# Kernel optimization log

Measured on AMD Instinct MI355X. Metric: run time of the kernel, lower is better.

## Reference

```python
import jax, jax.numpy as jnp
import numpy as np

EMBED = 1024

def setup_inputs() -> dict:
    key = jax.random.key(0)
    ks = jax.random.split(key, 10)
    B, S, E = 4, 2048, EMBED
    inv = 1.0 / np.sqrt(E)
    return {
        "query": jax.random.normal(ks[0], (B, S, E), jnp.float32),
        "key": jax.random.normal(ks[1], (B, S, E), jnp.float32),
        "value": jax.random.normal(ks[2], (B, S, E), jnp.float32),
        "attn_mask": jnp.zeros((B, S, S), jnp.float32),
        "Wq": jax.random.normal(ks[3], (E, E), jnp.float32) * inv,
        "bq": jnp.zeros((E,), jnp.float32),
        "Wk": jax.random.normal(ks[4], (E, E), jnp.float32) * inv,
        "bk": jnp.zeros((E,), jnp.float32),
        "Wv": jax.random.normal(ks[5], (E, E), jnp.float32) * inv,
        "bv": jnp.zeros((E,), jnp.float32),
    }

def reference(query, key, value, attn_mask, Wq, bq, Wk, bk, Wv, bv):
    E = query.shape[-1]
    q = query @ Wq.T + bq            # [B,S,E]
    k = key @ Wk.T + bk              # [B,S,E]
    v = value @ Wv.T + bv            # [B,S,E]
    scores = jnp.einsum('bse,bte->bst', q, k) / jnp.sqrt(jnp.float32(E))
    scores = scores + attn_mask      # [B,S,S]
    attn = jax.nn.softmax(scores, axis=-1)
    return jnp.einsum('bst,bte->bse', attn, v)
```

## Files before the change

### kernel.cpp

```cpp
#include <hip/hip_runtime.h>
#include <cstdint>
#include <cstddef>

typedef __bf16 bf16;
typedef __bf16 bf16x8 __attribute__((ext_vector_type(8)));
typedef float  f32x4  __attribute__((ext_vector_type(4)));

#define NB 4
#define SS 2048
#define EE 1024

#define BUFB   24576
#define LDS3   (3 * BUFB)
#define BUFB64 49152
#define LDS64  (3 * BUFB64)
#define LDS64P (LDS64 + 512)

static __device__ __forceinline__ void glds16(const bf16* g, void* l)
{
    __builtin_amdgcn_global_load_lds(
        (const __attribute__((address_space(1))) unsigned int*)g,
        (__attribute__((address_space(3))) unsigned int*)l,
        16, 0, 0);
}

static __device__ __forceinline__ void swz_block(int& bx, int& by, int& bz)
{
    const int nx = gridDim.x, ny = gridDim.y;
    const int nwg = nx * ny * gridDim.z;
    int lin = blockIdx.x + nx * (blockIdx.y + ny * blockIdx.z);
    const int per = nwg >> 3;
    lin = (lin & 7) * per + (lin >> 3);
    bz = lin / (nx * ny);
    const int r = lin - bz * nx * ny;
    by = r / nx;
    bx = r - by * nx;
}

static __device__ __forceinline__ void kloop32(
    const bf16* __restrict__ A, const bf16* __restrict__ Bm,
    int lda, int ldb, int nt, char* lds, int m0, int n0, int tid,
    f32x4 acc[4][4])
{
    constexpr int NBUF = 3;
    const int lane = tid & 63, w = tid >> 6;
    const int wm = w >> 2, wn = w & 3;
    const int lr = lane & 15, kq = lane >> 4;
    const int cb = ((kq ^ ((lr >> 1) & 3)) << 4);

    const int srow   = tid >> 2;
    const int chunkL = (tid & 3) ^ ((srow >> 1) & 3);
    const bf16* Asrc = A  + (size_t)(m0 + srow) * lda + chunkL * 8;
    const bf16* Bsrc = Bm + (size_t)(n0 + srow) * ldb + chunkL * 8;
    const int wofs = w << 10;

#pragma unroll
    for (int p = 0; p < NBUF - 1; ++p) {
        char* d = lds + p * BUFB + wofs;
        const int kt = p * 32;
        glds16(Asrc + kt,                     d);
        glds16(Bsrc + kt,                     d + 8192);
        glds16(Bsrc + (size_t)128 * ldb + kt, d + 16384);
    }
    asm volatile("s_waitcnt vmcnt(3)" ::: "memory");
    __builtin_amdgcn_sched_barrier(0);
    __builtin_amdgcn_s_barrier();
    __builtin_amdgcn_sched_barrier(0);

    int rb = 0, sb = NBUF - 1;
    for (int t = 0; t < nt; ++t) {
        char* la = lds + rb * BUFB;
        char* lb = la + 8192;
        const int ts = (t + NBUF - 1 < nt) ? t + NBUF - 1 : nt - 1;
        const int kt = ts * 32;
        char* d = lds + sb * BUFB + wofs;

        bf16x8 af[4], bg[4];
#pragma unroll
        for (int m = 0; m < 4; ++m)
            af[m] = *(const bf16x8*)(la + (wm * 64 + m * 16 + lr) * 64 + cb);
#pragma unroll
        for (int n = 0; n < 4; ++n)
            bg[n] = *(const bf16x8*)(lb + (wn * 64 + n * 16 + lr) * 64 + cb);

        glds16(Asrc + kt,                     d);
        glds16(Bsrc + kt,                     d + 8192);
        glds16(Bsrc + (size_t)128 * ldb + kt, d + 16384);

        __builtin_amdgcn_s_setprio(1);
#pragma unroll
        for (int m = 0; m < 4; ++m)
#pragma unroll
            for (int n = 0; n < 4; ++n)
                acc[m][n] = __builtin_amdgcn_mfma_f32_16x16x32_bf16(af[m], bg[n], acc[m][n], 0, 0, 0);
        __builtin_amdgcn_s_setprio(0);

        if (t < nt - 1) {
            asm volatile("s_waitcnt vmcnt(3)" ::: "memory");
            __builtin_amdgcn_sched_barrier(0);
            __builtin_amdgcn_s_barrier();
            __builtin_amdgcn_sched_barrier(0);
        }
        rb = (rb + 1 == NBUF) ? 0 : rb + 1;
        sb = (sb + 1 == NBUF) ? 0 : sb + 1;
    }
    asm volatile("s_waitcnt vmcnt(0)" ::: "memory");
}

static __device__ __forceinline__ void kloop32w(
    const bf16* __restrict__ A, const bf16* __restrict__ Bm,
    int lda, int ldb, int nt, char* lds, int m0, int n0, int tid,
    f32x4 acc[4][8])
{
    constexpr int NBUF = 3;
    const int lane = tid & 63, w = tid >> 6;
    const int wm = w >> 1, wn = w & 1;
    const int lr = lane & 15, kq = lane >> 4;
    const int cb = ((kq ^ ((lr >> 1) & 3)) << 4);

    const int srow   = tid >> 2;
    const int chunkL = (tid & 3) ^ ((srow >> 1) & 3);
    const bf16* Asrc = A  + (size_t)(m0 + srow) * lda + chunkL * 8;
    const bf16* Bsrc = Bm + (size_t)(n0 + srow) * ldb + chunkL * 8;
    const int wofs = w << 10;

#pragma unroll
    for (int p = 0; p < NBUF - 1; ++p) {
        char* d = lds + p * BUFB + wofs;
        const int kt = p * 32;
        glds16(Asrc + kt,                      d);
        glds16(Asrc + (size_t)64  * lda + kt,  d + 4096);
        glds16(Bsrc + kt,                      d + 8192);
        glds16(Bsrc + (size_t)64  * ldb + kt,  d + 12288);
        glds16(Bsrc + (size_t)128 * ldb + kt,  d + 16384);
        glds16(Bsrc + (size_t)192 * ldb + kt,  d + 20480);
    }
    asm volatile("s_waitcnt vmcnt(6)" ::: "memory");
    __builtin_amdgcn_sched_barrier(0);
    __builtin_amdgcn_s_barrier();
    __builtin_amdgcn_sched_barrier(0);

    int rb = 0, sb = NBUF - 1;
    for (int t = 0; t < nt; ++t) {
        char* la = lds + rb * BUFB;
        char* lb = la + 8192;
        const int ts = (t + NBUF - 1 < nt) ? t + NBUF - 1 : nt - 1;
        const int kt = ts * 32;
        char* d = lds + sb * BUFB + wofs;

        bf16x8 af[4], bg[8];
#pragma unroll
        for (int m = 0; m < 4; ++m)
            af[m] = *(const bf16x8*)(la + (wm * 64 + m * 16 + lr) * 64 + cb);
#pragma unroll
        for (int n = 0; n < 8; ++n)
            bg[n] = *(const bf16x8*)(lb + (wn * 128 + n * 16 + lr) * 64 + cb);

        glds16(Asrc + kt,                      d);
        glds16(Asrc + (size_t)64  * lda + kt,  d + 4096);
        glds16(Bsrc + kt,                      d + 8192);
        glds16(Bsrc + (size_t)64  * ldb + kt,  d + 12288);
        glds16(Bsrc + (size_t)128 * ldb + kt,  d + 16384);
        glds16(Bsrc + (size_t)192 * ldb + kt,  d + 20480);

        __builtin_amdgcn_s_setprio(1);
#pragma unroll
        for (int m = 0; m < 4; ++m)
#pragma unroll
            for (int n = 0; n < 8; ++n)
                acc[m][n] = __builtin_amdgcn_mfma_f32_16x16x32_bf16(af[m], bg[n], acc[m][n], 0, 0, 0);
        __builtin_amdgcn_s_setprio(0);

        if (t < nt - 1) {
            asm volatile("s_waitcnt vmcnt(6)" ::: "memory");
            __builtin_amdgcn_sched_barrier(0);
            __builtin_amdgcn_s_barrier();
            __builtin_amdgcn_sched_barrier(0);
        }
        rb = (rb + 1 == NBUF) ? 0 : rb + 1;
        sb = (sb + 1 == NBUF) ? 0 : sb + 1;
    }
    asm volatile("s_waitcnt vmcnt(0)" ::: "memory");
}

static __device__ __forceinline__ void kloop64(
    const bf16* __restrict__ A, const bf16* __restrict__ Bm,
    int lda, int ldb, int nt, char* lds, int m0, int n0, int tid,
    f32x4 acc[4][4])
{
    const int lane = tid & 63, w = tid >> 6;
    const int wm = w >> 2, wn = w & 3;
    const int lr = lane & 15, kq = lane >> 4;
    const int axor = (lr & 7) << 4;

    const int srow   = tid >> 3;
    const int chunkL = (tid & 7) ^ (srow & 7);
    const bf16* Asrc = A  + (size_t)(m0 + srow) * lda + chunkL * 8;
    const bf16* Bsrc = Bm + (size_t)(n0 + srow) * ldb + chunkL * 8;
    const int wofs = w << 10;

#pragma unroll
    for (int p = 0; p < 2; ++p) {
        char* d = lds + p * BUFB64 + wofs;
        const int kt = p * 64;
        glds16(Asrc + kt,                        d);
        glds16(Asrc + (size_t)64 * lda + kt,     d + 8192);
        glds16(Bsrc + kt,                        d + 16384);
        glds16(Bsrc + (size_t)64 * ldb + kt,     d + 16384 + 8192);
        glds16(Bsrc + (size_t)128 * ldb + kt,    d + 16384 + 16384);
        glds16(Bsrc + (size_t)192 * ldb + kt,    d + 16384 + 24576);
    }
    asm volatile("s_waitcnt vmcnt(6)" ::: "memory");
    __builtin_amdgcn_sched_barrier(0);
    __builtin_amdgcn_s_barrier();
    __builtin_amdgcn_sched_barrier(0);

    for (int t = 0; t < nt; ++t) {
        char* la = lds + (t % 3) * BUFB64;
        char* lb = la + 16384;
        char* sa = lds + ((t + 2) % 3) * BUFB64;
        const bool st = (t + 2) < nt;
        const int kt = (t + 2) * 64;

        bf16x8 af[4], bg[4];
        {
            const int cbk = (kq * 16) ^ axor;
#pragma unroll
            for (int m = 0; m < 4; ++m)
                af[m] = *(const bf16x8*)(la + (wm * 64 + m * 16 + lr) * 128 + cbk);
#pragma unroll
            for (int n = 0; n < 4; ++n)
                bg[n] = *(const bf16x8*)(lb + (wn * 64 + n * 16 + lr) * 128 + cbk);
            if (st) {
                glds16(Asrc + kt,                    sa + wofs);
                glds16(Asrc + (size_t)64 * lda + kt, sa + 8192 + wofs);
                glds16(Bsrc + kt,                    sa + 16384 + wofs);
            }
            __builtin_amdgcn_s_setprio(1);
#pragma unroll
            for (int m = 0; m < 4; ++m)
#pragma unroll
                for (int n = 0; n < 4; ++n)
                    acc[m][n] = __builtin_amdgcn_mfma_f32_16x16x32_bf16(af[m], bg[n], acc[m][n], 0, 0, 0);
            __builtin_amdgcn_s_setprio(0);
        }
        {
            const int cbk = (64 + kq * 16) ^ axor;
#pragma unroll
            for (int m = 0; m < 4; ++m)
                af[m] = *(const bf16x8*)(la + (wm * 64 + m * 16 + lr) * 128 + cbk);
#pragma unroll
            for (int n = 0; n < 4; ++n)
                bg[n] = *(const bf16x8*)(lb + (wn * 64 + n * 16 + lr) * 128 + cbk);
            if (st) {
                glds16(Bsrc + (size_t)64 * ldb + kt,  sa + 16384 + 8192 + wofs);
                glds16(Bsrc + (size_t)128 * ldb + kt, sa + 16384 + 16384 + wofs);
                glds16(Bsrc + (size_t)192 * ldb + kt, sa + 16384 + 24576 + wofs);
            }
            __builtin_amdgcn_s_setprio(1);
#pragma unroll
            for (int m = 0; m < 4; ++m)
#pragma unroll
                for (int n = 0; n < 4; ++n)
                    acc[m][n] = __builtin_amdgcn_mfma_f32_16x16x32_bf16(af[m], bg[n], acc[m][n], 0, 0, 0);
            __builtin_amdgcn_s_setprio(0);
        }
        if (t < nt - 1) {
            if (st) { asm volatile("s_waitcnt vmcnt(6)" ::: "memory"); }
            else    { asm volatile("s_waitcnt vmcnt(0)" ::: "memory"); }
            __builtin_amdgcn_sched_barrier(0);
            __builtin_amdgcn_s_barrier();
            __builtin_amdgcn_sched_barrier(0);
        }
    }
}

__global__ __launch_bounds__(256) void cvt_all(
    const float* __restrict__ q, const float* __restrict__ k, const float* __restrict__ v,
    const float* __restrict__ Wq, const float* __restrict__ Wk, const float* __restrict__ Wv,
    bf16* __restrict__ qc, bf16* __restrict__ kc, bf16* __restrict__ vc,
    bf16* __restrict__ Wc)
{
    const int y = blockIdx.y;
    const float* s; bf16* d; size_t i;
    if (blockIdx.x < 4096) {
        s = (y == 0) ? q : (y == 1) ? k : v;
        d = (y == 0) ? qc : (y == 1) ? kc : vc;
        i = ((size_t)blockIdx.x * 256 + threadIdx.x) * 8;
    } else {
        s = (y == 0) ? Wq : (y == 1) ? Wk : Wv;
        d = Wc + (size_t)y * EE * EE;
        i = ((size_t)(blockIdx.x - 4096) * 256 + threadIdx.x) * 8;
    }
    const float4 f0 = *(const float4*)(s + i);
    const float4 f1 = *(const float4*)(s + i + 4);
    bf16x8 h;
    h[0] = (bf16)f0.x; h[1] = (bf16)f0.y; h[2] = (bf16)f0.z; h[3] = (bf16)f0.w;
    h[4] = (bf16)f1.x; h[5] = (bf16)f1.y; h[6] = (bf16)f1.z; h[7] = (bf16)f1.w;
    *(bf16x8*)(d + i) = h;
}

__global__ __launch_bounds__(512, 4) void proj8(
    const bf16* __restrict__ qc, const bf16* __restrict__ kc, const bf16* __restrict__ vc,
    const bf16* __restrict__ Wc,
    const float* __restrict__ bq, const float* __restrict__ bk, const float* __restrict__ bv,
    bf16* __restrict__ qb, bf16* __restrict__ kb, bf16* __restrict__ vt)
{
    extern __shared__ char lds[];
    int bx, by, bz; swz_block(bx, by, bz);
    const bf16* A; const float* bias;
    if (bz == 0)      { A = qc; bias = bq; }
    else if (bz == 1) { A = kc; bias = bk; }
    else              { A = vc; bias = bv; }
    const bf16* Bm = Wc + (size_t)bz * EE * EE;

    const int m0 = by * 128, n0 = bx * 256;
    const int tid = threadIdx.x;

    f32x4 acc[4][4];
#pragma unroll
    for (int m = 0; m < 4; ++m)
#pragma unroll
        for (int n = 0; n < 4; ++n) { acc[m][n][0] = 0.f; acc[m][n][1] = 0.f; acc[m][n][2] = 0.f; acc[m][n][3] = 0.f; }

    kloop32(A, Bm, EE, EE, EE / 32, lds, m0, n0, tid, acc);

    const int lane = tid & 63, w = tid >> 6, wm = w >> 2, wn = w & 3;
    const int lr = lane & 15, kq = lane >> 4;

    if (bz < 2) {
        bf16* out = (bz == 0) ? qb : kb;
#pragma unroll
        for (int n = 0; n < 4; ++n) {
            const int gcol = n0 + wn * 64 + n * 16 + lr;
            const float bb = bias[gcol];
#pragma unroll
            for (int m = 0; m < 4; ++m)
#pragma unroll
                for (int j = 0; j < 4; ++j) {
                    const int grow = m0 + wm * 64 + m * 16 + kq * 4 + j;
                    out[(size_t)grow * EE + gcol] = (bf16)(acc[m][n][j] + bb);
                }
        }
    } else {
        __syncthreads();
#pragma unroll
        for (int n = 0; n < 4; ++n) {
            const int gc = wn * 64 + n * 16 + lr;
            const float bb = bias[n0 + gc];
#pragma unroll
            for (int m = 0; m < 4; ++m) {
                const int gr = wm * 64 + m * 16 + kq * 4;
                union { unsigned short u[4]; uint2 v; } h;
#pragma unroll
                for (int j = 0; j < 4; ++j) {
                    union { bf16 b; unsigned short u; } cv;
                    cv.b = (bf16)(acc[m][n][j] + bb);
                    h.u[j] = cv.u;
                }
                char* p = lds + gc * 256 + (((gr >> 3) ^ (gc & 7)) << 4) + (gr & 7) * 2;
                *(uint2*)p = h.v;
            }
        }
        __syncthreads();
        const int r = tid >> 1, par = tid & 1;
        const int bb_ = m0 >> 11;
        const int s0 = m0 & (SS - 1);
        bf16* dst = vt + ((size_t)bb_ * EE + n0 + r) * SS + s0 + par * 64;
#pragma unroll
        for (int i = 0; i < 8; ++i) {
            const int c = par * 8 + i;
            const char* p = lds + r * 256 + ((c ^ (r & 7)) << 4);
            *(uint4*)&dst[i * 8] = *(const uint4*)p;
        }
    }
}

__global__ __launch_bounds__(256, 2) void scores8(const bf16* __restrict__ qb,
                                                  const bf16* __restrict__ kb,
                                                  const float* __restrict__ mask,
                                                  bf16* __restrict__ sc,
                                                  float* __restrict__ part)
{
    extern __shared__ char lds[];
    int bx, by, bz; swz_block(bx, by, bz);
    const bf16* A  = qb + (size_t)bz * SS * EE;
    const bf16* Bm = kb + (size_t)bz * SS * EE;

    const int m0 = by * 128, n0 = bx * 256;
    const int tid = threadIdx.x;

    f32x4 acc[4][8];
#pragma unroll
    for (int m = 0; m < 4; ++m)
#pragma unroll
        for (int n = 0; n < 8; ++n) { acc[m][n][0] = 0.f; acc[m][n][1] = 0.f; acc[m][n][2] = 0.f; acc[m][n][3] = 0.f; }

    kloop32w(A, Bm, EE, EE, EE / 32, lds, m0, n0, tid, acc);

    const int lane = tid & 63, w = tid >> 6, wm = w >> 1, wn = w & 1;
    const int lr = lane & 15, kq = lane >> 4;
    const float* mrow = mask + (size_t)bz * SS * SS;
    bf16* out = sc + (size_t)bz * SS * SS;
    const float scale = 0.03125f;

    float rp[4][4];
#pragma unroll
    for (int m = 0; m < 4; ++m)
#pragma unroll
        for (int j = 0; j < 4; ++j) rp[m][j] = 0.f;

#pragma unroll
    for (int m = 0; m < 4; ++m)
#pragma unroll
        for (int n = 0; n < 8; ++n)
#pragma unroll
            for (int j = 0; j < 4; ++j) {
                const int grow = m0 + wm * 64 + m * 16 + kq * 4 + j;
                const int gcol = n0 + wn * 128 + n * 16 + lr;
                const float v = acc[m][n][j] * scale + mrow[(size_t)grow * SS + gcol];
                const float e = __expf(v);
                out[(size_t)grow * SS + gcol] = (bf16)e;
                rp[m][j] += e;
            }

#pragma unroll
    for (int m = 0; m < 4; ++m)
#pragma unroll
        for (int j = 0; j < 4; ++j) {
            float s = rp[m][j];
            s += __shfl_xor(s, 1);
            s += __shfl_xor(s, 2);
            s += __shfl_xor(s, 4);
            s += __shfl_xor(s, 8);
            rp[m][j] = s;
        }
    if (lr == 0) {
        float* pp = part + (size_t)(bx * 2 + wn) * (NB * SS) + (size_t)bz * SS + m0;
#pragma unroll
        for (int m = 0; m < 4; ++m)
#pragma unroll
            for (int j = 0; j < 4; ++j)
                pp[wm * 64 + m * 16 + kq * 4 + j] = rp[m][j];
    }
}

__global__ __launch_bounds__(512) void pv8(const bf16* __restrict__ sc,
                                           const bf16* __restrict__ vt,
                                           const float* __restrict__ part,
                                           float* __restrict__ outp)
{
    extern __shared__ char lds[];
    int bx, by, bz; swz_block(bx, by, bz);
    const bf16* A  = sc + (size_t)bz * SS * SS;
    const bf16* Bm = vt + (size_t)bz * EE * SS;

    const int m0 = by * 128, n0 = bx * 256;
    const int tid = threadIdx.x;

    float* invs = (float*)(lds + LDS64);
    if (tid < 128) {
        const size_t rowb = (size_t)bz * SS + m0 + tid;
        float s = 0.f;
#pragma unroll
        for (int i = 0; i < 16; ++i) s += part[(size_t)i * (NB * SS) + rowb];
        invs[tid] = 1.0f / s;
    }
    __syncthreads();

    f32x4 acc[4][4];
#pragma unroll
    for (int m = 0; m < 4; ++m)
#pragma unroll
        for (int n = 0; n < 4; ++n) { acc[m][n][0] = 0.f; acc[m][n][1] = 0.f; acc[m][n][2] = 0.f; acc[m][n][3] = 0.f; }

    kloop64(A, Bm, SS, SS, SS / 64, lds, m0, n0, tid, acc);

    const int lane = tid & 63, w = tid >> 6, wm = w >> 2, wn = w & 3;
    const int lr = lane & 15, kq = lane >> 4;
#pragma unroll
    for (int m = 0; m < 4; ++m)
#pragma unroll
        for (int j = 0; j < 4; ++j) {
            const int lrow = wm * 64 + m * 16 + kq * 4 + j;
            const float iv = invs[lrow];
#pragma unroll
            for (int n = 0; n < 4; ++n) {
                const int gcol = n0 + wn * 64 + n * 16 + lr;
                outp[((size_t)bz * SS + m0 + lrow) * EE + gcol] = acc[m][n][j] * iv;
            }
        }
}

extern "C" void kernel_launch(void* const* d_in, const int* in_sizes, int n_in,
                              void* d_out, int out_size, void* d_ws, size_t ws_size,
                              hipStream_t stream)
{
    const float* query = (const float*)d_in[0];
    const float* key_  = (const float*)d_in[1];
    const float* value = (const float*)d_in[2];
    const float* mask  = (const float*)d_in[3];
    const float* Wq = (const float*)d_in[4];
    const float* bq = (const float*)d_in[5];
    const float* Wk = (const float*)d_in[6];
    const float* bk = (const float*)d_in[7];
    const float* Wv = (const float*)d_in[8];
    const float* bv = (const float*)d_in[9];
    float* outp = (float*)d_out;

    char* ws = (char*)d_ws;
    const size_t QKV = (size_t)NB * SS * EE * 2;
    const size_t SCB = (size_t)NB * SS * SS * 2;
    const size_t WCB = (size_t)3 * EE * EE * 2;
    if (ws_size < 4 * QKV + SCB + WCB) return;

    bf16* qb = (bf16*)(ws);
    bf16* kb = (bf16*)(ws + QKV);
    bf16* vt = (bf16*)(ws + 3 * QKV);
    bf16* sc = (bf16*)(ws + 4 * QKV);
    bf16* Wc = (bf16*)(ws + 4 * QKV + SCB);
    bf16* qc = (bf16*)(ws + 2 * QKV);
    float* part = (float*)(ws + 2 * QKV);
    bf16* kc = sc;
    bf16* vc = (bf16*)(ws + 5 * QKV);

    (void)hipFuncSetAttribute((const void*)proj8,   hipFuncAttributeMaxDynamicSharedMemorySize, LDS3);
    (void)hipFuncSetAttribute((const void*)scores8, hipFuncAttributeMaxDynamicSharedMemorySize, LDS3);
    (void)hipFuncSetAttribute((const void*)pv8,     hipFuncAttributeMaxDynamicSharedMemorySize, LDS64P);

    dim3 blk(256), blk5(512);
    cvt_all<<<dim3(4096 + 512, 3), blk, 0, stream>>>(
        query, key_, value, Wq, Wk, Wv, qc, kc, vc, Wc);

    proj8<<<dim3(EE / 256, (NB * SS) / 128, 3), blk5, LDS3, stream>>>(
        qc, kc, vc, Wc, bq, bk, bv, qb, kb, vt);
    scores8<<<dim3(SS / 256, SS / 128, NB), blk, LDS3, stream>>>(qb, kb, mask, sc, part);
    pv8<<<dim3(EE / 256, SS / 128, NB), blk5, LDS64P, stream>>>(sc, vt, part, outp);
}
```

Baseline: 180.9 us.

## Fuse fp32-to-bf16 activation conversion into projection GEMM loads

Removes the separate conversion kernel for query/key/value and has the projection GEMM stream fp32 activations into LDS, converting to bf16 when loading MFMA fragments. This eliminates writing and re-reading a bf16 copy of the activations. In exchange the A tiles double in size, LDS per block grows to 96KB, the occupancy hint is dropped, and per-fragment conversion instructions are added to the inner loop.

```diff
diff --git a/kernel.cpp b/kernel.cpp
--- a/kernel.cpp
+++ b/kernel.cpp
@@ -12,11 +12,13 @@
 
 #define BUFB   24576
 #define LDS3   (3 * BUFB)
+#define BUFA32 32768
+#define LDSA3  (3 * BUFA32)
 #define BUFB64 49152
 #define LDS64  (3 * BUFB64)
 #define LDS64P (LDS64 + 512)
 
-static __device__ __forceinline__ void glds16(const bf16* g, void* l)
+static __device__ __forceinline__ void glds16(const void* g, void* l)
 {
     __builtin_amdgcn_global_load_lds(
         (const __attribute__((address_space(1))) unsigned int*)g,
@@ -37,8 +39,8 @@
     bx = r - by * nx;
 }
 
-static __device__ __forceinline__ void kloop32(
-    const bf16* __restrict__ A, const bf16* __restrict__ Bm,
+static __device__ __forceinline__ void kloop32a(
+    const float* __restrict__ A, const bf16* __restrict__ Bm,
     int lda, int ldb, int nt, char* lds, int m0, int n0, int tid,
     f32x4 acc[4][4])
 {
@@ -46,46 +48,59 @@
     const int lane = tid & 63, w = tid >> 6;
     const int wm = w >> 2, wn = w & 3;
     const int lr = lane & 15, kq = lane >> 4;
-    const int cb = ((kq ^ ((lr >> 1) & 3)) << 4);
-
-    const int srow   = tid >> 2;
-    const int chunkL = (tid & 3) ^ ((srow >> 1) & 3);
-    const bf16* Asrc = A  + (size_t)(m0 + srow) * lda + chunkL * 8;
-    const bf16* Bsrc = Bm + (size_t)(n0 + srow) * ldb + chunkL * 8;
+    const int cbB = ((kq ^ ((lr >> 1) & 3)) << 4);
+    const int ca0 = (((2 * kq)     ^ (lr & 7)) << 4);
+    const int ca1 = (((2 * kq + 1) ^ (lr & 7)) << 4);
+
+    const int arow = tid >> 3;
+    const int achk = (tid & 7) ^ (arow & 7);
+    const float* Asrc = A + (size_t)(m0 + arow) * lda + achk * 4;
+    const int brow = tid >> 2;
+    const int bchk = (tid & 3) ^ ((brow >> 1) & 3);
+    const bf16* Bsrc = Bm + (size_t)(n0 + brow) * ldb + bchk * 8;
     const int wofs = w << 10;
 
 #pragma unroll
     for (int p = 0; p < NBUF - 1; ++p) {
-        char* d = lds + p * BUFB + wofs;
+        char* d = lds + p * BUFA32;
         const int kt = p * 32;
-        glds16(Asrc + kt,                     d);
-        glds16(Bsrc + kt,                     d + 8192);
-        glds16(Bsrc + (size_t)128 * ldb + kt, d + 16384);
-    }
-    asm volatile("s_waitcnt vmcnt(3)" ::: "memory");
+        glds16(Asrc + kt,                     d + wofs);
+        glds16(Asrc + (size_t)64 * lda + kt,  d + 8192 + wofs);
+        glds16(Bsrc + kt,                     d + 16384 + wofs);
+        glds16(Bsrc + (size_t)128 * ldb + kt, d + 24576 + wofs);
+    }
+    asm volatile("s_waitcnt vmcnt(4)" ::: "memory");
     __builtin_amdgcn_sched_barrier(0);
     __builtin_amdgcn_s_barrier();
     __builtin_amdgcn_sched_barrier(0);
 
     int rb = 0, sb = NBUF - 1;
     for (int t = 0; t < nt; ++t) {
-        char* la = lds + rb * BUFB;
-        char* lb = la + 8192;
+        char* la = lds + rb * BUFA32;
+        char* lb = la + 16384;
         const int ts = (t + NBUF - 1 < nt) ? t + NBUF - 1 : nt - 1;
         const int kt = ts * 32;
-        char* d = lds + sb * BUFB + wofs;
+        char* d = lds + sb * BUFA32;
 
         bf16x8 af[4], bg[4];
 #pragma unroll
-        for (int m = 0; m < 4; ++m)
-            af[m] = *(const bf16x8*)(la + (wm * 64 + m * 16 + lr) * 64 + cb);
+        for (int m = 0; m < 4; ++m) {
+            const int r = wm * 64 + m * 16 + lr;
+            const f32x4 a0 = *(const f32x4*)(la + r * 128 + ca0);
+            const f32x4 a1 = *(const f32x4*)(la + r * 128 + ca1);
+            bf16x8 tf;
+            tf[0] = (bf16)a0[0]; tf[1] = (bf16)a0[1]; tf[2] = (bf16)a0[2]; tf[3] = (bf16)a0[3];
+            tf[4] = (bf16)a1[0]; tf[5] = (bf16)a1[1]; tf[6] = (bf16)a1[2]; tf[7] = (bf16)a1[3];
+            af[m] = tf;
+        }
 #pragma unroll
         for (int n = 0; n < 4; ++n)
-            bg[n] = *(const bf16x8*)(lb + (wn * 64 + n * 16 + lr) * 64 + cb);
-
-        glds16(Asrc + kt,                     d);
-        glds16(Bsrc + kt,                     d + 8192);
-        glds16(Bsrc + (size_t)128 * ldb + kt, d + 16384);
+            bg[n] = *(const bf16x8*)(lb + (wn * 64 + n * 16 + lr) * 64 + cbB);
+
+        glds16(Asrc + kt,                     d + wofs);
+        glds16(Asrc + (size_t)64 * lda + kt,  d + 8192 + wofs);
+        glds16(Bsrc + kt,                     d + 16384 + wofs);
+        glds16(Bsrc + (size_t)128 * ldb + kt, d + 24576 + wofs);
 
         __builtin_amdgcn_s_setprio(1);
 #pragma unroll
@@ -96,7 +111,7 @@
         __builtin_amdgcn_s_setprio(0);
 
         if (t < nt - 1) {
-            asm volatile("s_waitcnt vmcnt(3)" ::: "memory");
+            asm volatile("s_waitcnt vmcnt(4)" ::: "memory");
             __builtin_amdgcn_sched_barrier(0);
             __builtin_amdgcn_s_barrier();
             __builtin_amdgcn_sched_barrier(0);
@@ -275,23 +290,14 @@
     }
 }
 
-__global__ __launch_bounds__(256) void cvt_all(
-    const float* __restrict__ q, const float* __restrict__ k, const float* __restrict__ v,
+__global__ __launch_bounds__(256) void cvt_w(
     const float* __restrict__ Wq, const float* __restrict__ Wk, const float* __restrict__ Wv,
-    bf16* __restrict__ qc, bf16* __restrict__ kc, bf16* __restrict__ vc,
     bf16* __restrict__ Wc)
 {
     const int y = blockIdx.y;
-    const float* s; bf16* d; size_t i;
-    if (blockIdx.x < 4096) {
-        s = (y == 0) ? q : (y == 1) ? k : v;
-        d = (y == 0) ? qc : (y == 1) ? kc : vc;
-        i = ((size_t)blockIdx.x * 256 + threadIdx.x) * 8;
-    } else {
-        s = (y == 0) ? Wq : (y == 1) ? Wk : Wv;
-        d = Wc + (size_t)y * EE * EE;
-        i = ((size_t)(blockIdx.x - 4096) * 256 + threadIdx.x) * 8;
-    }
+    const float* s = (y == 0) ? Wq : (y == 1) ? Wk : Wv;
+    bf16* d = Wc + (size_t)y * EE * EE;
+    const size_t i = ((size_t)blockIdx.x * 256 + threadIdx.x) * 8;
     const float4 f0 = *(const float4*)(s + i);
     const float4 f1 = *(const float4*)(s + i + 4);
     bf16x8 h;
@@ -300,18 +306,19 @@
     *(bf16x8*)(d + i) = h;
 }
 
-__global__ __launch_bounds__(512, 4) void proj8(
-    const bf16* __restrict__ qc, const bf16* __restrict__ kc, const bf16* __restrict__ vc,
+__global__ __launch_bounds__(512) void proj8(
+    const float* __restrict__ query, const float* __restrict__ key_,
+    const float* __restrict__ value,
     const bf16* __restrict__ Wc,
     const float* __restrict__ bq, const float* __restrict__ bk, const float* __restrict__ bv,
     bf16* __restrict__ qb, bf16* __restrict__ kb, bf16* __restrict__ vt)
 {
     extern __shared__ char lds[];
     int bx, by, bz; swz_block(bx, by, bz);
-    const bf16* A; const float* bias;
-    if (bz == 0)      { A = qc; bias = bq; }
-    else if (bz == 1) { A = kc; bias = bk; }
-    else              { A = vc; bias = bv; }
+    const float* A; const float* bias;
+    if (bz == 0)      { A = query; bias = bq; }
+    else if (bz == 1) { A = key_;  bias = bk; }
+    else              { A = value; bias = bv; }
     const bf16* Bm = Wc + (size_t)bz * EE * EE;
 
     const int m0 = by * 128, n0 = bx * 256;
@@ -323,7 +330,7 @@
 #pragma unroll
         for (int n = 0; n < 4; ++n) { acc[m][n][0] = 0.f; acc[m][n][1] = 0.f; acc[m][n][2] = 0.f; acc[m][n][3] = 0.f; }
 
-    kloop32(A, Bm, EE, EE, EE / 32, lds, m0, n0, tid, acc);
+    kloop32a(A, Bm, EE, EE, EE / 32, lds, m0, n0, tid, acc);
 
     const int lane = tid & 63, w = tid >> 6, wm = w >> 2, wn = w & 3;
     const int lr = lane & 15, kq = lane >> 4;
@@ -516,24 +523,20 @@
 
     bf16* qb = (bf16*)(ws);
     bf16* kb = (bf16*)(ws + QKV);
+    float* part = (float*)(ws + 2 * QKV);
     bf16* vt = (bf16*)(ws + 3 * QKV);
     bf16* sc = (bf16*)(ws + 4 * QKV);
     bf16* Wc = (bf16*)(ws + 4 * QKV + SCB);
-    bf16* qc = (bf16*)(ws + 2 * QKV);
-    float* part = (float*)(ws + 2 * QKV);
-    bf16* kc = sc;
-    bf16* vc = (bf16*)(ws + 5 * QKV);
-
-    (void)hipFuncSetAttribute((const void*)proj8,   hipFuncAttributeMaxDynamicSharedMemorySize, LDS3);
+
+    (void)hipFuncSetAttribute((const void*)proj8,   hipFuncAttributeMaxDynamicSharedMemorySize, LDSA3);
     (void)hipFuncSetAttribute((const void*)scores8, hipFuncAttributeMaxDynamicSharedMemorySize, LDS3);
     (void)hipFuncSetAttribute((const void*)pv8,     hipFuncAttributeMaxDynamicSharedMemorySize, LDS64P);
 
     dim3 blk(256), blk5(512);
-    cvt_all<<<dim3(4096 + 512, 3), blk, 0, stream>>>(
-        query, key_, value, Wq, Wk, Wv, qc, kc, vc, Wc);
-
-    proj8<<<dim3(EE / 256, (NB * SS) / 128, 3), blk5, LDS3, stream>>>(
-        qc, kc, vc, Wc, bq, bk, bv, qb, kb, vt);
+    cvt_w<<<dim3(512, 3), blk, 0, stream>>>(Wq, Wk, Wv, Wc);
+
+    proj8<<<dim3(EE / 256, (NB * SS) / 128, 3), blk5, LDSA3, stream>>>(
+        query, key_, value, Wc, bq, bk, bv, qb, kb, vt);
     scores8<<<dim3(SS / 256, SS / 128, NB), blk, LDS3, stream>>>(qb, kb, mask, sc, part);
     pv8<<<dim3(EE / 256, SS / 128, NB), blk5, LDS64P, stream>>>(sc, vt, part, outp);
 }
```

Result: slower. 190.7 us (+5.4%).
